# Kernel optimization log

Measured on AMD Instinct MI355X. Metric: run time of the kernel, lower is better.

## Reference

```python
import jax, jax.numpy as jnp
import numpy as np

IN_F, OUT_F, STYLE_F = 512, 512, 256
B, N = 2, 131072


def setup_inputs() -> dict:
    key = jax.random.key(0)
    ks = jax.random.split(key, 5)
    x = jax.random.normal(ks[0], (B, N, IN_F), dtype=jnp.float32)
    z = jax.random.normal(ks[1], (B, STYLE_F), dtype=jnp.float32)
    # Parameters, initialized as in the torch module
    weight = jax.random.normal(ks[2], (OUT_F, IN_F), dtype=jnp.float32) / np.sqrt(IN_F)
    weight_alpha = jax.random.normal(ks[3], (IN_F, STYLE_F), dtype=jnp.float32) / np.sqrt(STYLE_F)
    bias_alpha = jnp.ones((IN_F,), dtype=jnp.float32)
    weight_beta = jax.random.normal(ks[4], (OUT_F, STYLE_F), dtype=jnp.float32) / np.sqrt(STYLE_F)
    bias_beta = jnp.zeros((OUT_F,), dtype=jnp.float32)
    return {"x": x, "z": z, "weight": weight, "weight_alpha": weight_alpha,
            "bias_alpha": bias_alpha, "weight_beta": weight_beta, "bias_beta": bias_beta}


def reference(x, z, weight, weight_alpha, bias_alpha, weight_beta, bias_beta):
    # ModLinear forward with bias=False, mod_bias=True, output_mode=True.
    # alpha: [B, in] style-derived input-channel modulation
    alpha = z @ weight_alpha.T + bias_alpha
    # beta: [B, out] style-derived output bias (output_mode=True)
    beta = z @ weight_beta.T + bias_beta
    # torch: w_mod = weight[None] * alpha[:, None, :]; out = baddbmm(beta, x, w_mod^T)
    # Equivalent fused form: (x * alpha) @ weight.T + beta, avoiding the [B,out,in] tensor.
    out = jnp.einsum('bni,oi->bno', x * alpha[:, None, :], weight) + beta[:, None, :]
    return out
```

## Files before the change

### kernel.cpp

```cpp
#include <hip/hip_runtime.h>

typedef __attribute__((ext_vector_type(4))) float f32x4;
typedef __attribute__((ext_vector_type(8))) short s16x8;
typedef __attribute__((ext_vector_type(8))) unsigned short u16x8;

#define IN_F 512
#define OUT_F 512
#define STYLE_F 256

__device__ __forceinline__ unsigned short f2bf(float f) {
    unsigned int u = __builtin_bit_cast(unsigned int, f);
    u += 0x7FFFu + ((u >> 16) & 1u);
    return (unsigned short)(u >> 16);
}

__global__ __launch_bounds__(256) void prep_kernel(
    const float* __restrict__ z,
    const float* __restrict__ weight,
    const float* __restrict__ w_alpha,
    const float* __restrict__ b_alpha,
    const float* __restrict__ w_beta,
    const float* __restrict__ b_beta,
    unsigned short* __restrict__ wfrag,
    float* __restrict__ alpha,
    float* __restrict__ beta)
{
    int gid = blockIdx.x * 256 + threadIdx.x;

    int f  = gid << 2;
    int e0 = f & 7;
    int l  = (f >> 3) & 63;
    int nf = (f >> 9) & 31;
    int ks = f >> 14;
    int n  = nf * 16 + (l & 15);
    int k  = ks * 32 + ((l >> 4) << 3) + e0;
    float4 wv = *reinterpret_cast<const float4*>(weight + n * IN_F + k);
    ushort4 o;
    o.x = f2bf(wv.x); o.y = f2bf(wv.y); o.z = f2bf(wv.z); o.w = f2bf(wv.w);
    *reinterpret_cast<ushort4*>(wfrag + f) = o;

    if (gid < 2048) {
        int t = gid & 1023;
        int b = t >> 9;
        int i = t & 511;
        const float* zr = z + b * STYLE_F;
        const float* wr = (gid < 1024 ? w_alpha : w_beta) + i * STYLE_F;
        float acc = 0.f;
        #pragma unroll 4
        for (int kk = 0; kk < STYLE_F; kk += 4) {
            float4 zv = *reinterpret_cast<const float4*>(zr + kk);
            float4 vv = *reinterpret_cast<const float4*>(wr + kk);
            acc += zv.x * vv.x + zv.y * vv.y + zv.z * vv.z + zv.w * vv.w;
        }
        if (gid < 1024) alpha[t] = acc + b_alpha[i];
        else            beta[t]  = acc + b_beta[i];
    }
}

__global__ __launch_bounds__(512, 2) void modlin_kernel(
    const float* __restrict__ x,
    const unsigned short* __restrict__ wfrag,
    const float* __restrict__ alpha,
    const float* __restrict__ beta,
    float* __restrict__ out)
{
    __shared__ __align__(16) unsigned short lds[2][128 * 64];

    const int tid = threadIdx.x;
    const int mb  = blockIdx.x;
    const long long row0 = (long long)mb * 128;
    const int b = mb >> 10;

    const int srow = tid >> 2;
    const int q    = tid & 3;
    const float* xs_base = x + (row0 + srow) * IN_F + q * 16;
    const float* al_base = alpha + b * IN_F + q * 16;
    const int wbyte0 = srow * 128 + (((2 * q    ) ^ (srow & 7)) << 4);
    const int wbyte1 = srow * 128 + (((2 * q + 1) ^ (srow & 7)) << 4);

    const int l  = tid & 63;
    const int w  = tid >> 6;
    const int wm = w >> 2;
    const int wn = w & 3;
    const int fr = l & 15;
    const int fq = l >> 4;
    const int arowbase = wm * 64 + fr;

    const unsigned short* bptr = wfrag + ((wn * 8) * 64 + l) * 8;

    f32x4 acc[4][8];
    #pragma unroll
    for (int i = 0; i < 4; i++)
        #pragma unroll
        for (int j = 0; j < 8; j++)
            acc[i][j] = (f32x4){0.f, 0.f, 0.f, 0.f};

    {
        float4 xv[4], av[4];
        #pragma unroll
        for (int u = 0; u < 4; u++) {
            xv[u] = *reinterpret_cast<const float4*>(xs_base + u * 4);
            av[u] = *reinterpret_cast<const float4*>(al_base + u * 4);
        }
        u16x8 h0, h1;
        #pragma unroll
        for (int u = 0; u < 2; u++) {
            h0[u * 4 + 0] = f2bf(xv[u].x * av[u].x);
            h0[u * 4 + 1] = f2bf(xv[u].y * av[u].y);
            h0[u * 4 + 2] = f2bf(xv[u].z * av[u].z);
            h0[u * 4 + 3] = f2bf(xv[u].w * av[u].w);
        }
        #pragma unroll
        for (int u = 2; u < 4; u++) {
            h1[(u - 2) * 4 + 0] = f2bf(xv[u].x * av[u].x);
            h1[(u - 2) * 4 + 1] = f2bf(xv[u].y * av[u].y);
            h1[(u - 2) * 4 + 2] = f2bf(xv[u].z * av[u].z);
            h1[(u - 2) * 4 + 3] = f2bf(xv[u].w * av[u].w);
        }
        char* lb = (char*)&lds[0][0];
        *reinterpret_cast<u16x8*>(lb + wbyte0) = h0;
        *reinterpret_cast<u16x8*>(lb + wbyte1) = h1;
    }

    for (int kt = 0; kt < 8; ++kt) {
        __syncthreads();
        char* cb = (char*)&lds[kt & 1][0];

        s16x8 afr[4];
        #pragma unroll
        for (int mf = 0; mf < 4; mf++) {
            int row  = arowbase + mf * 16;
            int byte = row * 128 + ((fq ^ (row & 7)) << 4);
            afr[mf] = *reinterpret_cast<const s16x8*>(cb + byte);
        }
        const unsigned short* bp0 = bptr + (kt * 2) * 16384;
        #pragma unroll
        for (int nf = 0; nf < 8; nf++) {
            s16x8 bf = *reinterpret_cast<const s16x8*>(bp0 + nf * 512);
            #pragma unroll
            for (int mf = 0; mf < 4; mf++)
                acc[mf][nf] = __builtin_amdgcn_mfma_f32_16x16x32_bf16(
                    afr[mf], bf, acc[mf][nf], 0, 0, 0);
        }

        float4 xv[4], av[4];
        if (kt < 7) {
            const float* xs = xs_base + (kt + 1) * 64;
            const float* as = al_base + (kt + 1) * 64;
            #pragma unroll
            for (int u = 0; u < 4; u++) {
                xv[u] = *reinterpret_cast<const float4*>(xs + u * 4);
                av[u] = *reinterpret_cast<const float4*>(as + u * 4);
            }
        }

        #pragma unroll
        for (int mf = 0; mf < 4; mf++) {
            int row  = arowbase + mf * 16;
            int byte = row * 128 + (((4 + fq) ^ (row & 7)) << 4);
            afr[mf] = *reinterpret_cast<const s16x8*>(cb + byte);
        }
        const unsigned short* bp1 = bp0 + 16384;
        #pragma unroll
        for (int nf = 0; nf < 8; nf++) {
            s16x8 bf = *reinterpret_cast<const s16x8*>(bp1 + nf * 512);
            #pragma unroll
            for (int mf = 0; mf < 4; mf++)
                acc[mf][nf] = __builtin_amdgcn_mfma_f32_16x16x32_bf16(
                    afr[mf], bf, acc[mf][nf], 0, 0, 0);
        }

        if (kt < 7) {
            u16x8 h0, h1;
            #pragma unroll
            for (int u = 0; u < 2; u++) {
                h0[u * 4 + 0] = f2bf(xv[u].x * av[u].x);
                h0[u * 4 + 1] = f2bf(xv[u].y * av[u].y);
                h0[u * 4 + 2] = f2bf(xv[u].z * av[u].z);
                h0[u * 4 + 3] = f2bf(xv[u].w * av[u].w);
            }
            #pragma unroll
            for (int u = 2; u < 4; u++) {
                h1[(u - 2) * 4 + 0] = f2bf(xv[u].x * av[u].x);
                h1[(u - 2) * 4 + 1] = f2bf(xv[u].y * av[u].y);
                h1[(u - 2) * 4 + 2] = f2bf(xv[u].z * av[u].z);
                h1[(u - 2) * 4 + 3] = f2bf(xv[u].w * av[u].w);
            }
            char* nb = (char*)&lds[(kt + 1) & 1][0];
            *reinterpret_cast<u16x8*>(nb + wbyte0) = h0;
            *reinterpret_cast<u16x8*>(nb + wbyte1) = h1;
        }
    }

    const float* brow = beta + b * OUT_F;
    #pragma unroll
    for (int nf = 0; nf < 8; nf++) {
        int col = wn * 128 + nf * 16 + fr;
        float bv = brow[col];
        #pragma unroll
        for (int mf = 0; mf < 4; mf++) {
            long long r = row0 + wm * 64 + mf * 16 + fq * 4;
            float* op = out + r * OUT_F + col;
            op[0 * OUT_F] = acc[mf][nf][0] + bv;
            op[1 * OUT_F] = acc[mf][nf][1] + bv;
            op[2 * OUT_F] = acc[mf][nf][2] + bv;
            op[3 * OUT_F] = acc[mf][nf][3] + bv;
        }
    }
}

extern "C" void kernel_launch(void* const* d_in, const int* in_sizes, int n_in,
                              void* d_out, int out_size, void* d_ws, size_t ws_size,
                              hipStream_t stream)
{
    const float* x       = (const float*)d_in[0];
    const float* z       = (const float*)d_in[1];
    const float* weight  = (const float*)d_in[2];
    const float* w_alpha = (const float*)d_in[3];
    const float* b_alpha = (const float*)d_in[4];
    const float* w_beta  = (const float*)d_in[5];
    const float* b_beta  = (const float*)d_in[6];
    float* out = (float*)d_out;

    unsigned short* wfrag = (unsigned short*)d_ws;
    float* alpha = (float*)((char*)d_ws + 512 * 1024);
    float* beta  = alpha + 2 * IN_F;

    prep_kernel<<<256, 256, 0, stream>>>(z, weight, w_alpha, b_alpha,
                                         w_beta, b_beta, wfrag, alpha, beta);
    modlin_kernel<<<2048, 512, 0, stream>>>(x, wfrag, alpha, beta, out);
}
```

Measured before the change: 336.9 us.

## Fold alpha into per-batch bf16 weights and stage full x rows in LDS

Alpha is now folded into a per-batch modulated bf16 weight fragment built in a separate prep kernel, so the main kernel no longer loads alpha or multiplies x by it. The main kernel switches from 128-row tiles with double-buffered 64-wide K chunks to 64-row tiles that load the whole 512-wide x row into LDS up front, then run all 16 K steps without further barriers. Occupancy target rises to 4 blocks of 512 threads per CU. The trade-off is no overlap between the global x load and the MFMA work inside a block (it relies on multiple resident blocks instead), one more prep launch, and twice the weight fragment storage.

Result: slower. 504.8 us (+49.8%).

```diff
diff --git a/kernel.cpp b/kernel.cpp
--- a/kernel.cpp
+++ b/kernel.cpp
@@ -14,20 +14,41 @@
     return (unsigned short)(u >> 16);
 }
 
-__global__ __launch_bounds__(256) void prep_kernel(
+__global__ __launch_bounds__(256) void prep1_kernel(
     const float* __restrict__ z,
-    const float* __restrict__ weight,
     const float* __restrict__ w_alpha,
     const float* __restrict__ b_alpha,
     const float* __restrict__ w_beta,
     const float* __restrict__ b_beta,
-    unsigned short* __restrict__ wfrag,
     float* __restrict__ alpha,
     float* __restrict__ beta)
 {
     int gid = blockIdx.x * 256 + threadIdx.x;
+    if (gid >= 2048) return;
+    int t = gid & 1023;
+    int b = t >> 9;
+    int i = t & 511;
+    const float* zr = z + b * STYLE_F;
+    const float* wr = (gid < 1024 ? w_alpha : w_beta) + i * STYLE_F;
+    float acc = 0.f;
+    #pragma unroll 4
+    for (int kk = 0; kk < STYLE_F; kk += 4) {
+        float4 zv = *reinterpret_cast<const float4*>(zr + kk);
+        float4 vv = *reinterpret_cast<const float4*>(wr + kk);
+        acc += zv.x * vv.x + zv.y * vv.y + zv.z * vv.z + zv.w * vv.w;
+    }
+    if (gid < 1024) alpha[t] = acc + b_alpha[i];
+    else            beta[t]  = acc + b_beta[i];
+}
 
-    int f  = gid << 2;
+__global__ __launch_bounds__(256) void prep2_kernel(
+    const float* __restrict__ weight,
+    const float* __restrict__ alpha,
+    unsigned short* __restrict__ wfragB)
+{
+    int gid = blockIdx.x * 256 + threadIdx.x;
+    int b = gid >> 16;
+    int f = (gid & 65535) << 2;
     int e0 = f & 7;
     int l  = (f >> 3) & 63;
     int nf = (f >> 9) & 31;
@@ -35,48 +56,51 @@
     int n  = nf * 16 + (l & 15);
     int k  = ks * 32 + ((l >> 4) << 3) + e0;
     float4 wv = *reinterpret_cast<const float4*>(weight + n * IN_F + k);
+    float4 av = *reinterpret_cast<const float4*>(alpha + b * IN_F + k);
     ushort4 o;
-    o.x = f2bf(wv.x); o.y = f2bf(wv.y); o.z = f2bf(wv.z); o.w = f2bf(wv.w);
-    *reinterpret_cast<ushort4*>(wfrag + f) = o;
-
-    if (gid < 2048) {
-        int t = gid & 1023;
-        int b = t >> 9;
-        int i = t & 511;
-        const float* zr = z + b * STYLE_F;
-        const float* wr = (gid < 1024 ? w_alpha : w_beta) + i * STYLE_F;
-        float acc = 0.f;
-        #pragma unroll 4
-        for (int kk = 0; kk < STYLE_F; kk += 4) {
-            float4 zv = *reinterpret_cast<const float4*>(zr + kk);
-            float4 vv = *reinterpret_cast<const float4*>(wr + kk);
-            acc += zv.x * vv.x + zv.y * vv.y + zv.z * vv.z + zv.w * vv.w;
-        }
-        if (gid < 1024) alpha[t] = acc + b_alpha[i];
-        else            beta[t]  = acc + b_beta[i];
-    }
+    o.x = f2bf(wv.x * av.x); o.y = f2bf(wv.y * av.y);
+    o.z = f2bf(wv.z * av.z); o.w = f2bf(wv.w * av.w);
+    *reinterpret_cast<ushort4*>(wfragB + b * 262144 + f) = o;
 }
 
-__global__ __launch_bounds__(512, 2) void modlin_kernel(
+__global__ __launch_bounds__(512, 4) void modlin_kernel(
     const float* __restrict__ x,
-    const unsigned short* __restrict__ wfrag,
-    const float* __restrict__ alpha,
+    const unsigned short* __restrict__ wfragB,
     const float* __restrict__ beta,
     float* __restrict__ out)
 {
-    __shared__ __align__(16) unsigned short lds[2][128 * 64];
+    __shared__ __align__(16) unsigned short lds[64 * 512];
 
     const int tid = threadIdx.x;
     const int mb  = blockIdx.x;
-    const long long row0 = (long long)mb * 128;
-    const int b = mb >> 10;
+    const long long row0 = (long long)mb * 64;
+    const int b = mb >> 11;
 
-    const int srow = tid >> 2;
-    const int q    = tid & 3;
-    const float* xs_base = x + (row0 + srow) * IN_F + q * 16;
-    const float* al_base = alpha + b * IN_F + q * 16;
-    const int wbyte0 = srow * 128 + (((2 * q    ) ^ (srow & 7)) << 4);
-    const int wbyte1 = srow * 128 + (((2 * q + 1) ^ (srow & 7)) << 4);
+    {
+        const int r = tid >> 3;
+        const int i = tid & 7;
+        const float* xr = x + (row0 + r) * IN_F + i * 8;
+        float4 v[16];
+        #pragma unroll
+        for (int c = 0; c < 8; c++) {
+            v[2 * c]     = *reinterpret_cast<const float4*>(xr + c * 64);
+            v[2 * c + 1] = *reinterpret_cast<const float4*>(xr + c * 64 + 4);
+        }
+        char* lb = (char*)lds;
+        const int rbase = r * 1024;
+        const int rx = r & 7;
+        #pragma unroll
+        for (int c = 0; c < 8; c++) {
+            u16x8 h;
+            h[0] = f2bf(v[2 * c].x);     h[1] = f2bf(v[2 * c].y);
+            h[2] = f2bf(v[2 * c].z);     h[3] = f2bf(v[2 * c].w);
+            h[4] = f2bf(v[2 * c + 1].x); h[5] = f2bf(v[2 * c + 1].y);
+            h[6] = f2bf(v[2 * c + 1].z); h[7] = f2bf(v[2 * c + 1].w);
+            int u = c * 8 + i;
+            *reinterpret_cast<u16x8*>(lb + rbase + ((u ^ rx) << 4)) = h;
+        }
+    }
+    __syncthreads();
 
     const int l  = tid & 63;
     const int w  = tid >> 6;
@@ -84,111 +108,35 @@
     const int wn = w & 3;
     const int fr = l & 15;
     const int fq = l >> 4;
-    const int arowbase = wm * 64 + fr;
 
-    const unsigned short* bptr = wfrag + ((wn * 8) * 64 + l) * 8;
+    const unsigned short* bbase = wfragB + (size_t)b * 262144
+                                + ((size_t)(wn * 8) * 64 + l) * 8;
 
-    f32x4 acc[4][8];
+    f32x4 acc[2][8];
     #pragma unroll
-    for (int i = 0; i < 4; i++)
+    for (int i = 0; i < 2; i++)
         #pragma unroll
         for (int j = 0; j < 8; j++)
             acc[i][j] = (f32x4){0.f, 0.f, 0.f, 0.f};
 
-    {
-        float4 xv[4], av[4];
-        #pragma unroll
-        for (int u = 0; u < 4; u++) {
-            xv[u] = *reinterpret_cast<const float4*>(xs_base + u * 4);
-            av[u] = *reinterpret_cast<const float4*>(al_base + u * 4);
-        }
-        u16x8 h0, h1;
-        #pragma unroll
-        for (int u = 0; u < 2; u++) {
-            h0[u * 4 + 0] = f2bf(xv[u].x * av[u].x);
-            h0[u * 4 + 1] = f2bf(xv[u].y * av[u].y);
-            h0[u * 4 + 2] = f2bf(xv[u].z * av[u].z);
-            h0[u * 4 + 3] = f2bf(xv[u].w * av[u].w);
-        }
-        #pragma unroll
-        for (int u = 2; u < 4; u++) {
-            h1[(u - 2) * 4 + 0] = f2bf(xv[u].x * av[u].x);
-            h1[(u - 2) * 4 + 1] = f2bf(xv[u].y * av[u].y);
-            h1[(u - 2) * 4 + 2] = f2bf(xv[u].z * av[u].z);
-            h1[(u - 2) * 4 + 3] = f2bf(xv[u].w * av[u].w);
-        }
-        char* lb = (char*)&lds[0][0];
-        *reinterpret_cast<u16x8*>(lb + wbyte0) = h0;
-        *reinterpret_cast<u16x8*>(lb + wbyte1) = h1;
-    }
+    const char* lb = (const char*)lds;
+    const int row0l = wm * 32 + fr;
+    const int row1l = row0l + 16;
+    const int sw0 = (row0l & 7) << 4;
+    const int sw1 = (row1l & 7) << 4;
+    const int rb0 = row0l * 1024;
+    const int rb1 = row1l * 1024;
 
-    for (int kt = 0; kt < 8; ++kt) {
-        __syncthreads();
-        char* cb = (char*)&lds[kt & 1][0];
-
-        s16x8 afr[4];
-        #pragma unroll
-        for (int mf = 0; mf < 4; mf++) {
-            int row  = arowbase + mf * 16;
-            int byte = row * 128 + ((fq ^ (row & 7)) << 4);
-            afr[mf] = *reinterpret_cast<const s16x8*>(cb + byte);
-        }
-        const unsigned short* bp0 = bptr + (kt * 2) * 16384;
+    for (int s = 0; s < 16; s++) {
+        const int ub = (s * 4 + fq) << 4;
+        s16x8 a0 = *reinterpret_cast<const s16x8*>(lb + rb0 + (ub ^ sw0));
+        s16x8 a1 = *reinterpret_cast<const s16x8*>(lb + rb1 + (ub ^ sw1));
+        const unsigned short* bp = bbase + s * 16384;
         #pragma unroll
         for (int nf = 0; nf < 8; nf++) {
-            s16x8 bf = *reinterpret_cast<const s16x8*>(bp0 + nf * 512);
-            #pragma unroll
-            for (int mf = 0; mf < 4; mf++)
-                acc[mf][nf] = __builtin_amdgcn_mfma_f32_16x16x32_bf16(
-                    afr[mf], bf, acc[mf][nf], 0, 0, 0);
-        }
-
-        float4 xv[4], av[4];
-        if (kt < 7) {
-            const float* xs = xs_base + (kt + 1) * 64;
-            const float* as = al_base + (kt + 1) * 64;
-            #pragma unroll
-            for (int u = 0; u < 4; u++) {
-                xv[u] = *reinterpret_cast<const float4*>(xs + u * 4);
-                av[u] = *reinterpret_cast<const float4*>(as + u * 4);
-            }
-        }
-
-        #pragma unroll
-        for (int mf = 0; mf < 4; mf++) {
-            int row  = arowbase + mf * 16;
-            int byte = row * 128 + (((4 + fq) ^ (row & 7)) << 4);
-            afr[mf] = *reinterpret_cast<const s16x8*>(cb + byte);
-        }
-        const unsigned short* bp1 = bp0 + 16384;
-        #pragma unroll
-        for (int nf = 0; nf < 8; nf++) {
-            s16x8 bf = *reinterpret_cast<const s16x8*>(bp1 + nf * 512);
-            #pragma unroll
-            for (int mf = 0; mf < 4; mf++)
-                acc[mf][nf] = __builtin_amdgcn_mfma_f32_16x16x32_bf16(
-                    afr[mf], bf, acc[mf][nf], 0, 0, 0);
-        }
-
-        if (kt < 7) {
-            u16x8 h0, h1;
-            #pragma unroll
-            for (int u = 0; u < 2; u++) {
-                h0[u * 4 + 0] = f2bf(xv[u].x * av[u].x);
-                h0[u * 4 + 1] = f2bf(xv[u].y * av[u].y);
-                h0[u * 4 + 2] = f2bf(xv[u].z * av[u].z);
-                h0[u * 4 + 3] = f2bf(xv[u].w * av[u].w);
-            }
-            #pragma unroll
-            for (int u = 2; u < 4; u++) {
-                h1[(u - 2) * 4 + 0] = f2bf(xv[u].x * av[u].x);
-                h1[(u - 2) * 4 + 1] = f2bf(xv[u].y * av[u].y);
-                h1[(u - 2) * 4 + 2] = f2bf(xv[u].z * av[u].z);
-                h1[(u - 2) * 4 + 3] = f2bf(xv[u].w * av[u].w);
-            }
-            char* nb = (char*)&lds[(kt + 1) & 1][0];
-            *reinterpret_cast<u16x8*>(nb + wbyte0) = h0;
-            *reinterpret_cast<u16x8*>(nb + wbyte1) = h1;
+            s16x8 bf = *reinterpret_cast<const s16x8*>(bp + nf * 512);
+            acc[0][nf] = __builtin_amdgcn_mfma_f32_16x16x32_bf16(a0, bf, acc[0][nf], 0, 0, 0);
+            acc[1][nf] = __builtin_amdgcn_mfma_f32_16x16x32_bf16(a1, bf, acc[1][nf], 0, 0, 0);
         }
     }
 
@@ -198,8 +146,8 @@
         int col = wn * 128 + nf * 16 + fr;
         float bv = brow[col];
         #pragma unroll
-        for (int mf = 0; mf < 4; mf++) {
-            long long r = row0 + wm * 64 + mf * 16 + fq * 4;
+        for (int mf = 0; mf < 2; mf++) {
+            long long r = row0 + wm * 32 + mf * 16 + fq * 4;
             float* op = out + r * OUT_F + col;
             op[0 * OUT_F] = acc[mf][nf][0] + bv;
             op[1 * OUT_F] = acc[mf][nf][1] + bv;
@@ -222,11 +170,12 @@
     const float* b_beta  = (const float*)d_in[6];
     float* out = (float*)d_out;
 
-    unsigned short* wfrag = (unsigned short*)d_ws;
-    float* alpha = (float*)((char*)d_ws + 512 * 1024);
+    unsigned short* wfragB = (unsigned short*)d_ws;
+    float* alpha = (float*)((char*)d_ws + 1048576);
     float* beta  = alpha + 2 * IN_F;
 
-    prep_kernel<<<256, 256, 0, stream>>>(z, weight, w_alpha, b_alpha,
-                                         w_beta, b_beta, wfrag, alpha, beta);
-    modlin_kernel<<<2048, 512, 0, stream>>>(x, wfrag, alpha, beta, out);
+    prep1_kernel<<<8, 256, 0, stream>>>(z, w_alpha, b_alpha, w_beta, b_beta,
+                                        alpha, beta);
+    prep2_kernel<<<512, 256, 0, stream>>>(weight, alpha, wfragB);
+    modlin_kernel<<<4096, 512, 0, stream>>>(x, wfragB, beta, out);
 }
```
